# Performance work log

Measured on AMD Instinct MI355X. Metric: run time of the kernel, lower is better.

Reference implementation:

```python
import jax, jax.numpy as jnp
import numpy as np

K = 3           # kernel_size
N_LAYERS = 2    # n_layers; circuit applies StronglyEntanglingLayers(weights) N_LAYERS times
STRIDE = 2
N_QUBITS = K * K  # 9 qubits -> 512-dim statevector


def _apply_1q(state, U, q):
    """Apply 2x2 unitary U (shared (2,2) or per-batch (P,2,2)) to qubit q.
    state: (P,) + (2,)*N_QUBITS complex64."""
    s = jnp.moveaxis(state, 1 + q, -1)
    if U.ndim == 3:
        s = jnp.einsum('pji,p...i->p...j', U, s)
    else:
        s = jnp.einsum('ji,...i->...j', U, s)
    return jnp.moveaxis(s, -1, 1 + q)


def _apply_cnot(state, c, t):
    """CNOT with control c, target t on state (P,)+(2,)*n."""
    s0 = jnp.take(state, 0, axis=1 + c)
    s1 = jnp.take(state, 1, axis=1 + c)
    t_ax = 1 + t if t < c else t  # target axis after control axis removed
    s1 = jnp.flip(s1, axis=t_ax)
    return jnp.stack([s0, s1], axis=1 + c)


def _rot_matrix(phi, theta, omega):
    """PennyLane Rot(phi, theta, omega) = RZ(omega) RY(theta) RZ(phi)."""
    c = jnp.cos(theta / 2)
    s = jnp.sin(theta / 2)
    u00 = jnp.exp(-0.5j * (phi + omega)) * c
    u01 = -jnp.exp(0.5j * (phi - omega)) * s
    u10 = jnp.exp(-0.5j * (phi - omega)) * s
    u11 = jnp.exp(0.5j * (phi + omega)) * c
    return jnp.stack([jnp.stack([u00, u01]), jnp.stack([u10, u11])]).astype(jnp.complex64)


def _circuit(angles, weights):
    """angles: (P, N_QUBITS) float32. Returns PauliZ expvals (P, N_QUBITS) float32."""
    P = angles.shape[0]
    n = N_QUBITS
    state = jnp.zeros((P, 2 ** n), jnp.complex64).at[:, 0].set(1.0)
    state = state.reshape((P,) + (2,) * n)
    # AngleEmbedding (default rotation = RX) per wire, angle varies per patch
    half = angles / 2
    cos = jnp.cos(half)
    sin = jnp.sin(half)
    for q in range(n):
        c = cos[:, q].astype(jnp.complex64)
        s = (-1j * sin[:, q]).astype(jnp.complex64)
        U = jnp.stack([jnp.stack([c, s], -1), jnp.stack([s, c], -1)], -2)  # (P,2,2)
        state = _apply_1q(state, U, q)
    # Faithful to source: StronglyEntanglingLayers(weights) applied N_LAYERS times,
    # each containing N_LAYERS internal layers (Rot on each wire + CNOT ring).
    for _ in range(N_LAYERS):
        for l in range(N_LAYERS):
            for q in range(n):
                state = _apply_1q(
                    state,
                    _rot_matrix(weights[l, q, 0], weights[l, q, 1], weights[l, q, 2]),
                    q,
                )
            r = (l % (n - 1)) + 1  # PennyLane default ranges
            for q in range(n):
                state = _apply_cnot(state, q, (q + r) % n)
    probs = state.real ** 2 + state.imag ** 2  # (P,)+(2,)*n
    exps = []
    for q in range(n):
        axes = tuple(ax for ax in range(1, n + 1) if ax != 1 + q)
        m = probs.sum(axis=axes)  # (P, 2)
        exps.append(m[:, 0] - m[:, 1])
    return jnp.stack(exps, axis=1)


def _forward(input, weights):
    B, _, H, W = input.shape
    out = (H - K) // STRIDE + 1
    starts = jnp.arange(out) * STRIDE
    win = starts[:, None] + jnp.arange(K)  # (out, K) row/col start offsets
    x = input[:, 0]  # (B, H, W), channels asserted == 1
    # vectorized sliding-window patch extraction: (B, out, out, K, K)
    patches = x[:, win[:, None, :, None], win[None, :, None, :]]
    angles = patches.reshape(B * out * out, N_QUBITS)  # row-major flatten, matches torch.flatten
    ev = _circuit(angles, weights)  # (B*out*out, N_QUBITS)
    ev = ev.reshape(B, out * out, N_QUBITS).transpose(0, 2, 1)
    return ev.reshape(B, N_QUBITS, out, out).astype(jnp.float32)


def setup_inputs() -> dict:
    key = jax.random.key(0)
    k1, k2 = jax.random.split(key)
    inp = jax.random.normal(k1, (8, 1, 128, 128), dtype=jnp.float32)
    weights = jax.random.uniform(k2, (N_LAYERS, N_QUBITS, 3), dtype=jnp.float32,
                                 minval=0.0, maxval=2 * np.pi)
    return {"input": inp, "weights": weights}


def reference(input, weights):
    return _forward(input, weights)
```

## Files before the change

### kernel.cpp

```cpp
#include <hip/hip_runtime.h>


namespace {

constexpr int OUT_HW = 63;
constexpr int PPB = 4;
constexpr int N_PATCH_TOTAL = 8 * OUT_HW * OUT_HW;

typedef _Float16 h2 __attribute__((ext_vector_type(2)));
typedef __fp16  hw2 __attribute__((ext_vector_type(2)));

__device__ __forceinline__ int h2i(h2 v) { return __builtin_bit_cast(int, v); }
__device__ __forceinline__ h2  i2h(int v) { return __builtin_bit_cast(h2, v); }
__device__ __forceinline__ h2  swap_h2(h2 v) { return __builtin_shufflevector(v, v, 1, 0); }

__device__ __forceinline__ int bperm_i(int addr, int v) {
    return __builtin_amdgcn_ds_bpermute(addr, v);
}

template<int M>
__device__ __forceinline__ int shfl_i(int v, int lane) {
    if constexpr (M < 32)
        return __builtin_amdgcn_ds_swizzle(v, 0x1F | (M << 10));
    else
        return bperm_i((lane << 2) ^ 128, v);
}
template<int M>
__device__ __forceinline__ float shfl_f(float v, int lane) {
    return __int_as_float(shfl_i<M>(__float_as_int(v), lane));
}

template<int C, int T>
__device__ __forceinline__ void cnot_h(h2 (&a)[8])
{
    constexpr int cm = 1 << C, tm = 1 << T;
    #pragma unroll
    for (int r = 0; r < 8; ++r) {
        if ((r & cm) && !(r & tm)) {
            const int r1 = r | tm;
            const h2 t = a[r]; a[r] = a[r1]; a[r1] = t;
        }
    }
}

__device__ __forceinline__ void ring1_partial_h(h2 (&a)[8], int lane)
{
    cnot_h<0,1>(a);
    cnot_h<1,2>(a);
    const int sA = (lane ^ ((lane & 31) << 1)) << 2;
    const int sB = sA ^ 4;
    #pragma unroll
    for (int r = 0; r < 8; ++r)
        a[r] = i2h(bperm_i((r & 4) ? sB : sA, h2i(a[r])));
}

__device__ __forceinline__ void ring2_partial_h(h2 (&a)[8], int lane)
{
    cnot_h<0,2>(a);
    const int s0 = (lane ^ ((lane & 15) << 2)) << 2;
    #pragma unroll
    for (int r = 0; r < 8; ++r) {
        const int ad = s0 ^ (((r >> 1) & 1) << 2) ^ (((r >> 2) & 1) << 3);
        a[r] = i2h(bperm_i(ad, h2i(a[r])));
    }
}

__device__ __forceinline__ void apply_diag_h(h2 (&a)[8],
                                             const int* __restrict__ dtab,
                                             int dbase, int lane)
{
    #pragma unroll
    for (int r = 0; r < 8; ++r) {
        const int idx = (dbase + r * 64 + lane) * 2;
        const h2 cc = i2h(dtab[idx]);
        const h2 ns = i2h(dtab[idx + 1]);
        a[r] = cc * a[r] + ns * swap_h2(a[r]);
    }
}

template<int QM>
__device__ __forceinline__ void regY_h(h2 (&a)[8], h2 A2, h2 B2, h2 C2, h2 D2)
{
    #pragma unroll
    for (int r = 0; r < 8; ++r) {
        if (!(r & QM)) {
            const int r1 = r | QM;
            const h2 x0 = a[r], x1 = a[r1];
            a[r]  = A2 * x0 + B2 * x1;
            a[r1] = C2 * x0 + D2 * x1;
        }
    }
}

template<int LM>
__device__ __forceinline__ void laneY_h(h2 (&a)[8], int lane, h2 c2, h2 sp2)
{
    #pragma unroll
    for (int r = 0; r < 8; ++r) {
        const h2 p = i2h(shfl_i<LM>(h2i(a[r]), lane));
        a[r] = c2 * a[r] + sp2 * p;
    }
}

__device__ __forceinline__ void apply_Y_h(h2 (&a)[8], int lane,
                                          const int* __restrict__ yt,
                                          bool sw0, bool sw1)
{
    {   const int cc = yt[0], ss = yt[1], ns = yt[2];
        regY_h<1>(a, i2h(sw0 ? ns : cc), i2h(sw0 ? cc : ns),
                     i2h(sw0 ? cc : ss), i2h(sw0 ? ss : cc)); }
    {   const int cc = yt[3], ss = yt[4], ns = yt[5];
        regY_h<2>(a, i2h(sw1 ? ns : cc), i2h(sw1 ? cc : ns),
                     i2h(sw1 ? cc : ss), i2h(sw1 ? ss : cc)); }
    {   regY_h<4>(a, i2h(yt[6]), i2h(yt[8]), i2h(yt[7]), i2h(yt[6])); }
    {   laneY_h<1>(a, lane, i2h(yt[9]),  i2h((lane & 1)        ? yt[10] : yt[11])); }
    {   laneY_h<2>(a, lane, i2h(yt[12]), i2h(((lane >> 1) & 1) ? yt[13] : yt[14])); }
    {   laneY_h<4>(a, lane, i2h(yt[15]), i2h(((lane >> 2) & 1) ? yt[16] : yt[17])); }
    {   laneY_h<8>(a, lane, i2h(yt[18]), i2h(((lane >> 3) & 1) ? yt[19] : yt[20])); }
    {   laneY_h<16>(a, lane, i2h(yt[21]), i2h(((lane >> 4) & 1) ? yt[22] : yt[23])); }
    {   laneY_h<32>(a, lane, i2h(yt[24]), i2h(((lane >> 5) & 1) ? yt[25] : yt[26])); }
}

__global__ void precomp_kernel(const float* __restrict__ w, float* __restrict__ ws)
{
    const int tid = threadIdx.x;
    float* rot = ws;
    int* ytab = (int*)(ws + 144);
    int* dtab = (int*)(ws + 208);
    if (tid < 18) {
        const float phi = w[tid*3 + 0], theta = w[tid*3 + 1], omega = w[tid*3 + 2];
        const float ct = cosf(0.5f * theta), st = sinf(0.5f * theta);
        const float apo = 0.5f * (phi + omega), amo = 0.5f * (phi - omega);
        const float ca = cosf(apo), sa = sinf(apo);
        const float cm = cosf(amo), sm = sinf(amo);
        float* m = rot + tid * 8;
        m[0] =  ca * ct; m[1] = -sa * ct;
        m[2] = -cm * st; m[3] = -sm * st;
        m[4] =  cm * st; m[5] = -sm * st;
        m[6] =  ca * ct; m[7] =  sa * ct;
        h2 cc; cc.x = (_Float16)ct;  cc.y = (_Float16)ct;
        h2 ss; ss.x = (_Float16)st;  ss.y = (_Float16)st;
        h2 ns; ns.x = (_Float16)(-st); ns.y = (_Float16)(-st);
        ytab[tid*3 + 0] = h2i(cc);
        ytab[tid*3 + 1] = h2i(ss);
        ytab[tid*3 + 2] = h2i(ns);
    }
    if (tid < 192) {
        const int vmask[9] = {0x1FE,0x003,0x007,0x00F,0x01F,0x03F,0x07F,0x0FF,0x1FF};
        const int wmask[9] = {0x0AB,0x157,0x005,0x00A,0x015,0x02A,0x055,0x0AA,0x155};
        const int d = tid >> 6, lane = tid & 63;
        for (int r = 0; r < 8; ++r) {
            const int p = (lane << 3) | r;
            float ang = 0.f;
            for (int q = 0; q < 9; ++q) {
                if (d == 0) {
                    const float lam = -0.5f * w[(9 + q)*3 + 0];
                    ang += (__popc(p & vmask[q]) & 1) ? -lam : lam;
                } else if (d == 1) {
                    const float lam = -0.5f * w[q*3 + 0];
                    ang += (__popc(p & wmask[q]) & 1) ? -lam : lam;
                    const float lm2 = -0.5f * w[(9 + q)*3 + 2];
                    ang += ((p >> q) & 1) ? -lm2 : lm2;
                } else {
                    const float lam = -0.5f * w[(9 + q)*3 + 0];
                    ang += (__popc(p & vmask[q]) & 1) ? -lam : lam;
                    const float lm2 = -0.5f * w[q*3 + 2];
                    ang += ((p >> q) & 1) ? -lm2 : lm2;
                }
            }
            const float c = cosf(ang), s = sinf(ang);
            h2 cc;  cc.x = (_Float16)c;    cc.y = (_Float16)c;
            h2 nsp; nsp.x = (_Float16)(-s); nsp.y = (_Float16)s;
            const int idx = ((d*8 + r)*64 + lane)*2;
            dtab[idx + 0] = h2i(cc);
            dtab[idx + 1] = h2i(nsp);
        }
    }
}

__device__ __forceinline__ float sgn_apply(float v, int par) {
    return __int_as_float(__float_as_int(v) ^ (par << 31));
}

__global__ __launch_bounds__(PPB * 64, 8) void qconv_kernel(
    const float* __restrict__ x,
    const float* __restrict__ ws,
    float* __restrict__ out)
{
    const float* rot  = ws;
    const int* ytab = (const int*)(ws + 144);
    const int* dtab = (const int*)(ws + 208);

    const int lane  = threadIdx.x & 63;
    const int wv    = threadIdx.x >> 6;
    const int patch = blockIdx.x * PPB + wv;

    const int b   = patch / (OUT_HW * OUT_HW);
    const int rem = patch - b * (OUT_HW * OUT_HW);
    const int oy  = rem / OUT_HW;
    const int ox  = rem - oy * OUT_HW;

    __shared__ float abtab[PPB][36];
    {
        const int t = threadIdx.x;
        if (t < PPB * 36) {
            const int tw = t / 36, j = t - tw * 36;
            const int q = j >> 2, comp = j & 3;
            const int tp   = blockIdx.x * PPB + tw;
            const int tb   = tp / (OUT_HW * OUT_HW);
            const int trem = tp - tb * (OUT_HW * OUT_HW);
            const int toy  = trem / OUT_HW;
            const int tox  = trem - toy * OUT_HW;
            const float ang = x[tb * 16384 + (toy * 2 + q / 3) * 128 + (tox * 2 + q % 3)];
            float s, c;
            __sincosf(0.5f * ang, &s, &c);
            const float* R = rot + 8 * q;
            float v;
            if      (comp == 0) v = c*R[0] + s*R[3];
            else if (comp == 1) v = c*R[1] - s*R[2];
            else if (comp == 2) v = c*R[4] + s*R[7];
            else                v = c*R[5] - s*R[6];
            abtab[tw][j] = v;
        }
    }
    __syncthreads();

    float ab[36];
    {
        const float4* src = reinterpret_cast<const float4*>(&abtab[wv][0]);
        float4* dst = reinterpret_cast<float4*>(ab);
        #pragma unroll
        for (int j = 0; j < 9; ++j) dst[j] = src[j];
    }

    float ar[8], ai[8];
    {
        float Lr = 1.0f, Li = 0.0f;
        #pragma unroll
        for (int q = 3; q < 9; ++q) {
            const int bit = (lane >> (q - 3)) & 1;
            const float fr = bit ? ab[4*q + 2] : ab[4*q + 0];
            const float fi = bit ? ab[4*q + 3] : ab[4*q + 1];
            const float nr = Lr*fr - Li*fi;
            const float ni = Lr*fi + Li*fr;
            Lr = nr; Li = ni;
        }
        float c01r[4], c01i[4];
        #pragma unroll
        for (int j = 0; j < 4; ++j) {
            const float f0r = (j & 1) ? ab[2] : ab[0];
            const float f0i = (j & 1) ? ab[3] : ab[1];
            const float f1r = (j & 2) ? ab[6] : ab[4];
            const float f1i = (j & 2) ? ab[7] : ab[5];
            c01r[j] = f0r*f1r - f0i*f1i;
            c01i[j] = f0r*f1i + f0i*f1r;
        }
        float hr[4], hi[4];
        #pragma unroll
        for (int j = 0; j < 4; ++j) {
            hr[j] = c01r[j]*Lr - c01i[j]*Li;
            hi[j] = c01r[j]*Li + c01i[j]*Lr;
        }
        #pragma unroll
        for (int r = 0; r < 8; ++r) {
            const float f2r = (r & 4) ? ab[10] : ab[8];
            const float f2i = (r & 4) ? ab[11] : ab[9];
            ar[r] = hr[r & 3]*f2r - hi[r & 3]*f2i;
            ai[r] = hr[r & 3]*f2i + hi[r & 3]*f2r;
        }
    }

    h2 a[8];
    #pragma unroll
    for (int r = 0; r < 8; ++r)
        a[r] = __builtin_bit_cast(h2, __builtin_amdgcn_cvt_pkrtz(ar[r], ai[r]));

    const bool b4 = ((lane >> 4) & 1) != 0;
    const bool b5 = ((lane >> 5) & 1) != 0;

    apply_diag_h(a, dtab, 0 * 512, lane);
    ring1_partial_h(a, lane);
    apply_Y_h(a, lane, ytab + 27, b5, false);
    apply_diag_h(a, dtab, 1 * 512, lane);
    ring2_partial_h(a, lane);
    apply_Y_h(a, lane, ytab + 0, b4, b5);
    apply_diag_h(a, dtab, 2 * 512, lane);
    ring1_partial_h(a, lane);
    apply_Y_h(a, lane, ytab + 27, b5, false);

    float p[8];
    #pragma unroll
    for (int r = 0; r < 8; ++r) {
#if __has_builtin(__builtin_amdgcn_fdot2)
        p[r] = __builtin_amdgcn_fdot2(__builtin_bit_cast(hw2, a[r]),
                                      __builtin_bit_cast(hw2, a[r]), 0.0f, false);
#else
        const float xr = (float)a[r].x, xi = (float)a[r].y;
        p[r] = xr*xr + xi*xi;
#endif
    }

    const float t03 = p[0]+p[3], t12 = p[1]+p[2], t47 = p[4]+p[7], t56 = p[5]+p[6];
    float S3 = (t03 + t47) - (t12 + t56);
    float S7 = (t03 + t56) - (t12 + t47);
    const float u02 = p[0]+p[2], u13 = p[1]+p[3], u57 = p[5]+p[7], u46 = p[4]+p[6];
    float S5 = (u02 + u57) - (u13 + u46);
    const float v01 = p[0]+p[1], v23 = p[2]+p[3], v45 = p[4]+p[5], v67 = p[6]+p[7];
    float S2 = (v01 + v45) - (v23 + v67);

    const int sm0 = (lane & 1) << 31;
    const int sm1 = ((lane >> 1) & 1) << 31;
    const int sm2 = ((lane >> 2) & 1) << 31;
    const int sm3 = ((lane >> 3) & 1) << 31;
    const int sm4 = ((lane >> 4) & 1) << 31;
    const int sm5 = ((lane >> 5) & 1) << 31;
#define WHT_STAGE(M, SM) { \
    const float q3 = shfl_f<M>(S3, lane), q7 = shfl_f<M>(S7, lane); \
    const float q5 = shfl_f<M>(S5, lane), q2 = shfl_f<M>(S2, lane); \
    S3 = q3 + __int_as_float(__float_as_int(S3) ^ (SM)); \
    S7 = q7 + __int_as_float(__float_as_int(S7) ^ (SM)); \
    S5 = q5 + __int_as_float(__float_as_int(S5) ^ (SM)); \
    S2 = q2 + __int_as_float(__float_as_int(S2) ^ (SM)); }
    WHT_STAGE(1,  sm0)
    WHT_STAGE(2,  sm1)
    WHT_STAGE(4,  sm2)
    WHT_STAGE(8,  sm3)
    WHT_STAGE(16, sm4)
    WHT_STAGE(32, sm5)
#undef WHT_STAGE

    const int base = b * 9;
    const int pix  = oy * OUT_HW + ox;
    int chA = -1; float vA = 0.f;
    if (lane == 0x00) { chA = 2; vA = S5; }
    if (lane == 0x02) { chA = 4; vA = S5; }
    if (lane == 0x0A) { chA = 6; vA = S5; }
    if (lane == 0x2A) { chA = 8; vA = S5; }
    if (lane == 0x01) { chA = 3; vA = S2; }
    if (lane == 0x05) { chA = 5; vA = S2; }
    if (lane == 0x15) { chA = 7; vA = S2; }
    if (chA >= 0)
        out[(base + chA) * (OUT_HW * OUT_HW) + pix] = vA;
    if (lane == 0x15)
        out[(base + 0) * (OUT_HW * OUT_HW) + pix] = S3;
    if (lane == 0x2A)
        out[(base + 1) * (OUT_HW * OUT_HW) + pix] = S7;
}

}

extern "C" void kernel_launch(void* const* d_in, const int* in_sizes, int n_in,
                              void* d_out, int out_size, void* d_ws, size_t ws_size,
                              hipStream_t stream)
{
    const float* x = (const float*)d_in[0];
    const float* w = (const float*)d_in[1];
    float* ws = (float*)d_ws;
    float* out = (float*)d_out;

    precomp_kernel<<<1, 256, 0, stream>>>(w, ws);
    qconv_kernel<<<N_PATCH_TOTAL / PPB, PPB * 64, 0, stream>>>(x, ws, out);
}
```

Before: 110.0 us.

## Compute per-wave angle tables locally, use wave barrier, prefetch diagonal tables

Each wave now computes its own 36 rotation coefficients and synchronizes with a wave barrier instead of a block-wide __syncthreads. The block size drops from four to two patches per block. The next diagonal-phase table is prefetched into registers before the ring and Y stages so its global loads overlap with that compute. The cost is more registers held live, which could lower occupancy.

```diff
diff --git a/kernel.cpp b/kernel.cpp
--- a/kernel.cpp
+++ b/kernel.cpp
@@ -4,7 +4,7 @@
 namespace {
 
 constexpr int OUT_HW = 63;
-constexpr int PPB = 4;
+constexpr int PPB = 2;
 constexpr int N_PATCH_TOTAL = 8 * OUT_HW * OUT_HW;
 
 typedef _Float16 h2 __attribute__((ext_vector_type(2)));
@@ -76,6 +76,27 @@
         const h2 ns = i2h(dtab[idx + 1]);
         a[r] = cc * a[r] + ns * swap_h2(a[r]);
     }
+}
+
+__device__ __forceinline__ void load_diag(h2 (&cc)[8], h2 (&ns)[8],
+                                          const int* __restrict__ dtab,
+                                          int dbase, int lane)
+{
+    #pragma unroll
+    for (int r = 0; r < 8; ++r) {
+        const int idx = (dbase + r * 64 + lane) * 2;
+        cc[r] = i2h(dtab[idx]);
+        ns[r] = i2h(dtab[idx + 1]);
+    }
+}
+
+__device__ __forceinline__ void apply_diag_pre(h2 (&a)[8],
+                                               const h2 (&cc)[8],
+                                               const h2 (&ns)[8])
+{
+    #pragma unroll
+    for (int r = 0; r < 8; ++r)
+        a[r] = cc[r] * a[r] + ns[r] * swap_h2(a[r]);
 }
 
 template<int QM>
@@ -178,10 +199,6 @@
     }
 }
 
-__device__ __forceinline__ float sgn_apply(float v, int par) {
-    return __int_as_float(__float_as_int(v) ^ (par << 31));
-}
-
 __global__ __launch_bounds__(PPB * 64, 8) void qconv_kernel(
     const float* __restrict__ x,
     const float* __restrict__ ws,
@@ -200,30 +217,21 @@
     const int oy  = rem / OUT_HW;
     const int ox  = rem - oy * OUT_HW;
 
-    __shared__ float abtab[PPB][36];
-    {
-        const int t = threadIdx.x;
-        if (t < PPB * 36) {
-            const int tw = t / 36, j = t - tw * 36;
-            const int q = j >> 2, comp = j & 3;
-            const int tp   = blockIdx.x * PPB + tw;
-            const int tb   = tp / (OUT_HW * OUT_HW);
-            const int trem = tp - tb * (OUT_HW * OUT_HW);
-            const int toy  = trem / OUT_HW;
-            const int tox  = trem - toy * OUT_HW;
-            const float ang = x[tb * 16384 + (toy * 2 + q / 3) * 128 + (tox * 2 + q % 3)];
-            float s, c;
-            __sincosf(0.5f * ang, &s, &c);
-            const float* R = rot + 8 * q;
-            float v;
-            if      (comp == 0) v = c*R[0] + s*R[3];
-            else if (comp == 1) v = c*R[1] - s*R[2];
-            else if (comp == 2) v = c*R[4] + s*R[7];
-            else                v = c*R[5] - s*R[6];
-            abtab[tw][j] = v;
-        }
-    }
-    __syncthreads();
+    __shared__ __align__(16) float abtab[PPB][36];
+    if (lane < 36) {
+        const int q = lane >> 2, comp = lane & 3;
+        const float ang = x[b * 16384 + (oy * 2 + q / 3) * 128 + (ox * 2 + q % 3)];
+        float s, c;
+        __sincosf(0.5f * ang, &s, &c);
+        const float* R = rot + 8 * q;
+        float v;
+        if      (comp == 0) v = c*R[0] + s*R[3];
+        else if (comp == 1) v = c*R[1] - s*R[2];
+        else if (comp == 2) v = c*R[4] + s*R[7];
+        else                v = c*R[5] - s*R[6];
+        abtab[wv][lane] = v;
+    }
+    __builtin_amdgcn_wave_barrier();
 
     float ab[36];
     {
@@ -278,13 +286,16 @@
     const bool b4 = ((lane >> 4) & 1) != 0;
     const bool b5 = ((lane >> 5) & 1) != 0;
 
+    h2 dcc[8], dns[8];
     apply_diag_h(a, dtab, 0 * 512, lane);
+    load_diag(dcc, dns, dtab, 1 * 512, lane);
     ring1_partial_h(a, lane);
     apply_Y_h(a, lane, ytab + 27, b5, false);
-    apply_diag_h(a, dtab, 1 * 512, lane);
+    apply_diag_pre(a, dcc, dns);
+    load_diag(dcc, dns, dtab, 2 * 512, lane);
     ring2_partial_h(a, lane);
     apply_Y_h(a, lane, ytab + 0, b4, b5);
-    apply_diag_h(a, dtab, 2 * 512, lane);
+    apply_diag_pre(a, dcc, dns);
     ring1_partial_h(a, lane);
     apply_Y_h(a, lane, ytab + 27, b5, false);
 
```

Result: no change. 112.2 us (+1.9%).

## Pack two patches per wavefront with 16 amplitudes per lane

Applied to the files above, without the earlier changes.

Each 64-lane wavefront now simulates two patches, one per 32-lane half, and each lane holds 16 amplitudes instead of 8. Qubit-to-lane/register mappings, CNOT permutations, the diagonal-table layout, the Walsh-Hadamard reduction and the output lane selection are all remapped to match. The block-wide barrier becomes a wave barrier. The aim is to halve the number of wavefronts and cut cross-lane shuffles per amplitude. The cost is more registers per lane and lower occupancy (launch bounds reduced to 4), plus the risk of errors in the remapped qubit indexing.

```diff
diff --git a/kernel.cpp b/kernel.cpp
--- a/kernel.cpp
+++ b/kernel.cpp
@@ -4,8 +4,9 @@
 namespace {
 
 constexpr int OUT_HW = 63;
-constexpr int PPB = 4;
-constexpr int N_PATCH_TOTAL = 8 * OUT_HW * OUT_HW;
+constexpr int N_PIX = OUT_HW * OUT_HW;
+constexpr int PPB = 2;
+constexpr int N_PATCH_TOTAL = 8 * N_PIX;
 
 typedef _Float16 h2 __attribute__((ext_vector_type(2)));
 typedef __fp16  hw2 __attribute__((ext_vector_type(2)));
@@ -31,11 +32,11 @@
 }
 
 template<int C, int T>
-__device__ __forceinline__ void cnot_h(h2 (&a)[8])
+__device__ __forceinline__ void cnot16(h2 (&a)[16])
 {
     constexpr int cm = 1 << C, tm = 1 << T;
     #pragma unroll
-    for (int r = 0; r < 8; ++r) {
+    for (int r = 0; r < 16; ++r) {
         if ((r & cm) && !(r & tm)) {
             const int r1 = r | tm;
             const h2 t = a[r]; a[r] = a[r1]; a[r1] = t;
@@ -43,46 +44,51 @@
     }
 }
 
-__device__ __forceinline__ void ring1_partial_h(h2 (&a)[8], int lane)
-{
-    cnot_h<0,1>(a);
-    cnot_h<1,2>(a);
-    const int sA = (lane ^ ((lane & 31) << 1)) << 2;
+__device__ __forceinline__ void ring1_partial16(h2 (&a)[16], int lane)
+{
+    cnot16<0,1>(a);
+    cnot16<1,2>(a);
+    cnot16<2,3>(a);
+    const int l5 = lane & 31;
+    const int hi = (lane & 32) << 2;
+    const int sA = ((l5 ^ ((l5 & 15) << 1)) << 2) | hi;
     const int sB = sA ^ 4;
     #pragma unroll
-    for (int r = 0; r < 8; ++r)
-        a[r] = i2h(bperm_i((r & 4) ? sB : sA, h2i(a[r])));
-}
-
-__device__ __forceinline__ void ring2_partial_h(h2 (&a)[8], int lane)
-{
-    cnot_h<0,2>(a);
-    const int s0 = (lane ^ ((lane & 15) << 2)) << 2;
-    #pragma unroll
-    for (int r = 0; r < 8; ++r) {
-        const int ad = s0 ^ (((r >> 1) & 1) << 2) ^ (((r >> 2) & 1) << 3);
+    for (int r = 0; r < 16; ++r)
+        a[r] = i2h(bperm_i((r & 8) ? sB : sA, h2i(a[r])));
+}
+
+__device__ __forceinline__ void ring2_partial16(h2 (&a)[16], int lane)
+{
+    cnot16<0,2>(a);
+    cnot16<1,3>(a);
+    const int l5 = lane & 31;
+    const int s0 = ((l5 ^ ((l5 & 7) << 2)) << 2) | ((lane & 32) << 2);
+    #pragma unroll
+    for (int r = 0; r < 16; ++r) {
+        const int ad = s0 ^ (((r >> 3) & 1) << 3) ^ (((r >> 2) & 1) << 2);
         a[r] = i2h(bperm_i(ad, h2i(a[r])));
     }
 }
 
-__device__ __forceinline__ void apply_diag_h(h2 (&a)[8],
+__device__ __forceinline__ void apply_diag16(h2 (&a)[16],
                                              const int* __restrict__ dtab,
-                                             int dbase, int lane)
-{
-    #pragma unroll
-    for (int r = 0; r < 8; ++r) {
-        const int idx = (dbase + r * 64 + lane) * 2;
-        const h2 cc = i2h(dtab[idx]);
-        const h2 ns = i2h(dtab[idx + 1]);
+                                             int dbase, int lane5)
+{
+    const int* dp = dtab + (dbase + (lane5 << 4)) * 2;
+    #pragma unroll
+    for (int r = 0; r < 16; ++r) {
+        const h2 cc = i2h(dp[2 * r]);
+        const h2 ns = i2h(dp[2 * r + 1]);
         a[r] = cc * a[r] + ns * swap_h2(a[r]);
     }
 }
 
 template<int QM>
-__device__ __forceinline__ void regY_h(h2 (&a)[8], h2 A2, h2 B2, h2 C2, h2 D2)
-{
-    #pragma unroll
-    for (int r = 0; r < 8; ++r) {
+__device__ __forceinline__ void regY16(h2 (&a)[16], h2 A2, h2 B2, h2 C2, h2 D2)
+{
+    #pragma unroll
+    for (int r = 0; r < 16; ++r) {
         if (!(r & QM)) {
             const int r1 = r | QM;
             const h2 x0 = a[r], x1 = a[r1];
@@ -93,32 +99,32 @@
 }
 
 template<int LM>
-__device__ __forceinline__ void laneY_h(h2 (&a)[8], int lane, h2 c2, h2 sp2)
-{
-    #pragma unroll
-    for (int r = 0; r < 8; ++r) {
+__device__ __forceinline__ void laneY16(h2 (&a)[16], int lane, h2 c2, h2 sp2)
+{
+    #pragma unroll
+    for (int r = 0; r < 16; ++r) {
         const h2 p = i2h(shfl_i<LM>(h2i(a[r]), lane));
         a[r] = c2 * a[r] + sp2 * p;
     }
 }
 
-__device__ __forceinline__ void apply_Y_h(h2 (&a)[8], int lane,
+__device__ __forceinline__ void apply_Y16(h2 (&a)[16], int lane,
                                           const int* __restrict__ yt,
                                           bool sw0, bool sw1)
 {
     {   const int cc = yt[0], ss = yt[1], ns = yt[2];
-        regY_h<1>(a, i2h(sw0 ? ns : cc), i2h(sw0 ? cc : ns),
+        regY16<1>(a, i2h(sw0 ? ns : cc), i2h(sw0 ? cc : ns),
                      i2h(sw0 ? cc : ss), i2h(sw0 ? ss : cc)); }
     {   const int cc = yt[3], ss = yt[4], ns = yt[5];
-        regY_h<2>(a, i2h(sw1 ? ns : cc), i2h(sw1 ? cc : ns),
+        regY16<2>(a, i2h(sw1 ? ns : cc), i2h(sw1 ? cc : ns),
                      i2h(sw1 ? cc : ss), i2h(sw1 ? ss : cc)); }
-    {   regY_h<4>(a, i2h(yt[6]), i2h(yt[8]), i2h(yt[7]), i2h(yt[6])); }
-    {   laneY_h<1>(a, lane, i2h(yt[9]),  i2h((lane & 1)        ? yt[10] : yt[11])); }
-    {   laneY_h<2>(a, lane, i2h(yt[12]), i2h(((lane >> 1) & 1) ? yt[13] : yt[14])); }
-    {   laneY_h<4>(a, lane, i2h(yt[15]), i2h(((lane >> 2) & 1) ? yt[16] : yt[17])); }
-    {   laneY_h<8>(a, lane, i2h(yt[18]), i2h(((lane >> 3) & 1) ? yt[19] : yt[20])); }
-    {   laneY_h<16>(a, lane, i2h(yt[21]), i2h(((lane >> 4) & 1) ? yt[22] : yt[23])); }
-    {   laneY_h<32>(a, lane, i2h(yt[24]), i2h(((lane >> 5) & 1) ? yt[25] : yt[26])); }
+    {   regY16<4>(a, i2h(yt[6]),  i2h(yt[8]),  i2h(yt[7]),  i2h(yt[6])); }
+    {   regY16<8>(a, i2h(yt[9]),  i2h(yt[11]), i2h(yt[10]), i2h(yt[9])); }
+    {   laneY16<1> (a, lane, i2h(yt[12]), i2h((lane & 1)        ? yt[13] : yt[14])); }
+    {   laneY16<2> (a, lane, i2h(yt[15]), i2h(((lane >> 1) & 1) ? yt[16] : yt[17])); }
+    {   laneY16<4> (a, lane, i2h(yt[18]), i2h(((lane >> 2) & 1) ? yt[19] : yt[20])); }
+    {   laneY16<8> (a, lane, i2h(yt[21]), i2h(((lane >> 3) & 1) ? yt[22] : yt[23])); }
+    {   laneY16<16>(a, lane, i2h(yt[24]), i2h(((lane >> 4) & 1) ? yt[25] : yt[26])); }
 }
 
 __global__ void precomp_kernel(const float* __restrict__ w, float* __restrict__ ws)
@@ -148,9 +154,9 @@
     if (tid < 192) {
         const int vmask[9] = {0x1FE,0x003,0x007,0x00F,0x01F,0x03F,0x07F,0x0FF,0x1FF};
         const int wmask[9] = {0x0AB,0x157,0x005,0x00A,0x015,0x02A,0x055,0x0AA,0x155};
-        const int d = tid >> 6, lane = tid & 63;
+        const int d = tid >> 6, ln = tid & 63;
         for (int r = 0; r < 8; ++r) {
-            const int p = (lane << 3) | r;
+            const int p = (ln << 3) | r;
             float ang = 0.f;
             for (int q = 0; q < 9; ++q) {
                 if (d == 0) {
@@ -171,18 +177,14 @@
             const float c = cosf(ang), s = sinf(ang);
             h2 cc;  cc.x = (_Float16)c;    cc.y = (_Float16)c;
             h2 nsp; nsp.x = (_Float16)(-s); nsp.y = (_Float16)s;
-            const int idx = ((d*8 + r)*64 + lane)*2;
+            const int idx = (d * 512 + p) * 2;
             dtab[idx + 0] = h2i(cc);
             dtab[idx + 1] = h2i(nsp);
         }
     }
 }
 
-__device__ __forceinline__ float sgn_apply(float v, int par) {
-    return __int_as_float(__float_as_int(v) ^ (par << 31));
-}
-
-__global__ __launch_bounds__(PPB * 64, 8) void qconv_kernel(
+__global__ __launch_bounds__(PPB * 64, 4) void qconv_kernel(
     const float* __restrict__ x,
     const float* __restrict__ ws,
     float* __restrict__ out)
@@ -191,27 +193,23 @@
     const int* ytab = (const int*)(ws + 144);
     const int* dtab = (const int*)(ws + 208);
 
-    const int lane  = threadIdx.x & 63;
-    const int wv    = threadIdx.x >> 6;
-    const int patch = blockIdx.x * PPB + wv;
-
-    const int b   = patch / (OUT_HW * OUT_HW);
-    const int rem = patch - b * (OUT_HW * OUT_HW);
-    const int oy  = rem / OUT_HW;
-    const int ox  = rem - oy * OUT_HW;
-
-    __shared__ float abtab[PPB][36];
+    const int lane   = threadIdx.x & 63;
+    const int wv     = threadIdx.x >> 6;
+    const int lane5  = lane & 31;
+    const int half   = lane >> 5;
+    const int patch2 = (blockIdx.x * PPB + wv) * 2;
+
+    __shared__ __align__(16) float abtab[PPB][2][36];
     {
-        const int t = threadIdx.x;
-        if (t < PPB * 36) {
-            const int tw = t / 36, j = t - tw * 36;
+        auto stage_val = [&](int h, int j) {
             const int q = j >> 2, comp = j & 3;
-            const int tp   = blockIdx.x * PPB + tw;
-            const int tb   = tp / (OUT_HW * OUT_HW);
-            const int trem = tp - tb * (OUT_HW * OUT_HW);
+            const int tp   = patch2 + h;
+            const int tb   = tp / N_PIX;
+            const int trem = tp - tb * N_PIX;
             const int toy  = trem / OUT_HW;
             const int tox  = trem - toy * OUT_HW;
-            const float ang = x[tb * 16384 + (toy * 2 + q / 3) * 128 + (tox * 2 + q % 3)];
+            const int qr = q / 3, qc = q - 3 * qr;
+            const float ang = x[tb * 16384 + (toy * 2 + qr) * 128 + (tox * 2 + qc)];
             float s, c;
             __sincosf(0.5f * ang, &s, &c);
             const float* R = rot + 8 * q;
@@ -220,77 +218,85 @@
             else if (comp == 1) v = c*R[1] - s*R[2];
             else if (comp == 2) v = c*R[4] + s*R[7];
             else                v = c*R[5] - s*R[6];
-            abtab[tw][j] = v;
-        }
-    }
-    __syncthreads();
+            abtab[wv][h][j] = v;
+        };
+        const int h1 = (lane >= 36) ? 1 : 0;
+        stage_val(h1, lane - 36 * h1);
+        if (lane < 8) stage_val(1, 28 + lane);
+    }
+    __builtin_amdgcn_wave_barrier();
 
     float ab[36];
     {
-        const float4* src = reinterpret_cast<const float4*>(&abtab[wv][0]);
+        const float4* src = reinterpret_cast<const float4*>(&abtab[wv][half][0]);
         float4* dst = reinterpret_cast<float4*>(ab);
         #pragma unroll
         for (int j = 0; j < 9; ++j) dst[j] = src[j];
     }
 
-    float ar[8], ai[8];
+    h2 a[16];
     {
-        float Lr = 1.0f, Li = 0.0f;
-        #pragma unroll
-        for (int q = 3; q < 9; ++q) {
-            const int bit = (lane >> (q - 3)) & 1;
+        float Lr, Li;
+        {
+            const int bit = lane5 & 1;
+            Lr = ab[16 + (bit ? 2 : 0)];
+            Li = ab[16 + (bit ? 3 : 1)];
+        }
+        #pragma unroll
+        for (int q = 5; q <= 8; ++q) {
+            const int bit = (lane5 >> (q - 4)) & 1;
             const float fr = bit ? ab[4*q + 2] : ab[4*q + 0];
             const float fi = bit ? ab[4*q + 3] : ab[4*q + 1];
             const float nr = Lr*fr - Li*fi;
             const float ni = Lr*fi + Li*fr;
             Lr = nr; Li = ni;
         }
-        float c01r[4], c01i[4];
+        float c01r[4], c01i[4], c23r[4], c23i[4];
         #pragma unroll
         for (int j = 0; j < 4; ++j) {
-            const float f0r = (j & 1) ? ab[2] : ab[0];
-            const float f0i = (j & 1) ? ab[3] : ab[1];
-            const float f1r = (j & 2) ? ab[6] : ab[4];
-            const float f1i = (j & 2) ? ab[7] : ab[5];
+            const float f0r = (j & 1) ? ab[2]  : ab[0];
+            const float f0i = (j & 1) ? ab[3]  : ab[1];
+            const float f1r = (j & 2) ? ab[6]  : ab[4];
+            const float f1i = (j & 2) ? ab[7]  : ab[5];
             c01r[j] = f0r*f1r - f0i*f1i;
             c01i[j] = f0r*f1i + f0i*f1r;
-        }
-        float hr[4], hi[4];
+            const float g2r = (j & 1) ? ab[10] : ab[8];
+            const float g2i = (j & 1) ? ab[11] : ab[9];
+            const float g3r = (j & 2) ? ab[14] : ab[12];
+            const float g3i = (j & 2) ? ab[15] : ab[13];
+            c23r[j] = g2r*g3r - g2i*g3i;
+            c23i[j] = g2r*g3i + g2i*g3r;
+        }
+        float hlr[4], hli[4];
         #pragma unroll
         for (int j = 0; j < 4; ++j) {
-            hr[j] = c01r[j]*Lr - c01i[j]*Li;
-            hi[j] = c01r[j]*Li + c01i[j]*Lr;
-        }
-        #pragma unroll
-        for (int r = 0; r < 8; ++r) {
-            const float f2r = (r & 4) ? ab[10] : ab[8];
-            const float f2i = (r & 4) ? ab[11] : ab[9];
-            ar[r] = hr[r & 3]*f2r - hi[r & 3]*f2i;
-            ai[r] = hr[r & 3]*f2i + hi[r & 3]*f2r;
-        }
-    }
-
-    h2 a[8];
-    #pragma unroll
-    for (int r = 0; r < 8; ++r)
-        a[r] = __builtin_bit_cast(h2, __builtin_amdgcn_cvt_pkrtz(ar[r], ai[r]));
-
-    const bool b4 = ((lane >> 4) & 1) != 0;
-    const bool b5 = ((lane >> 5) & 1) != 0;
-
-    apply_diag_h(a, dtab, 0 * 512, lane);
-    ring1_partial_h(a, lane);
-    apply_Y_h(a, lane, ytab + 27, b5, false);
-    apply_diag_h(a, dtab, 1 * 512, lane);
-    ring2_partial_h(a, lane);
-    apply_Y_h(a, lane, ytab + 0, b4, b5);
-    apply_diag_h(a, dtab, 2 * 512, lane);
-    ring1_partial_h(a, lane);
-    apply_Y_h(a, lane, ytab + 27, b5, false);
-
-    float p[8];
-    #pragma unroll
-    for (int r = 0; r < 8; ++r) {
+            hlr[j] = c01r[j]*Lr - c01i[j]*Li;
+            hli[j] = c01r[j]*Li + c01i[j]*Lr;
+        }
+        #pragma unroll
+        for (int r = 0; r < 16; ++r) {
+            const float fr = hlr[r & 3]*c23r[r >> 2] - hli[r & 3]*c23i[r >> 2];
+            const float fi = hlr[r & 3]*c23i[r >> 2] + hli[r & 3]*c23r[r >> 2];
+            a[r] = __builtin_bit_cast(h2, __builtin_amdgcn_cvt_pkrtz(fr, fi));
+        }
+    }
+
+    const bool q7b = ((lane >> 3) & 1) != 0;
+    const bool q8b = ((lane >> 4) & 1) != 0;
+
+    apply_diag16(a, dtab, 0 * 512, lane5);
+    ring1_partial16(a, lane);
+    apply_Y16(a, lane, ytab + 27, q8b, false);
+    apply_diag16(a, dtab, 1 * 512, lane5);
+    ring2_partial16(a, lane);
+    apply_Y16(a, lane, ytab + 0, q7b, q8b);
+    apply_diag16(a, dtab, 2 * 512, lane5);
+    ring1_partial16(a, lane);
+    apply_Y16(a, lane, ytab + 27, q8b, false);
+
+    float p[16];
+    #pragma unroll
+    for (int r = 0; r < 16; ++r) {
 #if __has_builtin(__builtin_amdgcn_fdot2)
         p[r] = __builtin_amdgcn_fdot2(__builtin_bit_cast(hw2, a[r]),
                                       __builtin_bit_cast(hw2, a[r]), 0.0f, false);
@@ -300,51 +306,66 @@
 #endif
     }
 
-    const float t03 = p[0]+p[3], t12 = p[1]+p[2], t47 = p[4]+p[7], t56 = p[5]+p[6];
-    float S3 = (t03 + t47) - (t12 + t56);
-    float S7 = (t03 + t56) - (t12 + t47);
-    const float u02 = p[0]+p[2], u13 = p[1]+p[3], u57 = p[5]+p[7], u46 = p[4]+p[6];
-    float S5 = (u02 + u57) - (u13 + u46);
-    const float v01 = p[0]+p[1], v23 = p[2]+p[3], v45 = p[4]+p[5], v67 = p[6]+p[7];
-    float S2 = (v01 + v45) - (v23 + v67);
+    float A[8], B[8];
+    #pragma unroll
+    for (int j = 0; j < 8; ++j) {
+        A[j] = p[2*j] + p[2*j+1];
+        B[j] = p[2*j] - p[2*j+1];
+    }
+    float P5[4], P7[4], P10[4];
+    #pragma unroll
+    for (int k = 0; k < 4; ++k) {
+        P5[k]  = B[2*k] + B[2*k+1];
+        P7[k]  = B[2*k] - B[2*k+1];
+        P10[k] = A[2*k] - A[2*k+1];
+    }
+    float S5  = (P5[0]  - P5[1])  + (P5[2]  - P5[3]);
+    float S7  = (P7[0]  - P7[1])  + (P7[2]  - P7[3]);
+    float S11 = (P7[0]  + P7[1])  - (P7[2]  + P7[3]);
+    float S10 = (P10[0] + P10[1]) - (P10[2] + P10[3]);
 
     const int sm0 = (lane & 1) << 31;
     const int sm1 = ((lane >> 1) & 1) << 31;
     const int sm2 = ((lane >> 2) & 1) << 31;
     const int sm3 = ((lane >> 3) & 1) << 31;
     const int sm4 = ((lane >> 4) & 1) << 31;
-    const int sm5 = ((lane >> 5) & 1) << 31;
 #define WHT_STAGE(M, SM) { \
-    const float q3 = shfl_f<M>(S3, lane), q7 = shfl_f<M>(S7, lane); \
-    const float q5 = shfl_f<M>(S5, lane), q2 = shfl_f<M>(S2, lane); \
-    S3 = q3 + __int_as_float(__float_as_int(S3) ^ (SM)); \
-    S7 = q7 + __int_as_float(__float_as_int(S7) ^ (SM)); \
-    S5 = q5 + __int_as_float(__float_as_int(S5) ^ (SM)); \
-    S2 = q2 + __int_as_float(__float_as_int(S2) ^ (SM)); }
+    const float qa = shfl_f<M>(S5, lane),  qb = shfl_f<M>(S7, lane); \
+    const float qc = shfl_f<M>(S10, lane), qd = shfl_f<M>(S11, lane); \
+    S5  = qa + __int_as_float(__float_as_int(S5)  ^ (SM)); \
+    S7  = qb + __int_as_float(__float_as_int(S7)  ^ (SM)); \
+    S10 = qc + __int_as_float(__float_as_int(S10) ^ (SM)); \
+    S11 = qd + __int_as_float(__float_as_int(S11) ^ (SM)); }
     WHT_STAGE(1,  sm0)
     WHT_STAGE(2,  sm1)
     WHT_STAGE(4,  sm2)
     WHT_STAGE(8,  sm3)
     WHT_STAGE(16, sm4)
-    WHT_STAGE(32, sm5)
 #undef WHT_STAGE
 
+    const int patch = patch2 + half;
+    const int b   = patch / N_PIX;
+    const int rem = patch - b * N_PIX;
+    const int oy  = rem / OUT_HW;
+    const int ox  = rem - oy * OUT_HW;
     const int base = b * 9;
     const int pix  = oy * OUT_HW + ox;
-    int chA = -1; float vA = 0.f;
-    if (lane == 0x00) { chA = 2; vA = S5; }
-    if (lane == 0x02) { chA = 4; vA = S5; }
-    if (lane == 0x0A) { chA = 6; vA = S5; }
-    if (lane == 0x2A) { chA = 8; vA = S5; }
-    if (lane == 0x01) { chA = 3; vA = S2; }
-    if (lane == 0x05) { chA = 5; vA = S2; }
-    if (lane == 0x15) { chA = 7; vA = S2; }
-    if (chA >= 0)
-        out[(base + chA) * (OUT_HW * OUT_HW) + pix] = vA;
-    if (lane == 0x15)
-        out[(base + 0) * (OUT_HW * OUT_HW) + pix] = S3;
-    if (lane == 0x2A)
-        out[(base + 1) * (OUT_HW * OUT_HW) + pix] = S7;
+
+    if (lane5 == 0x00) {
+        out[(base + 2) * N_PIX + pix] = S5;
+        out[(base + 3) * N_PIX + pix] = S10;
+    }
+    if (lane5 == 0x01) out[(base + 4) * N_PIX + pix] = S5;
+    if (lane5 == 0x02) out[(base + 5) * N_PIX + pix] = S10;
+    if (lane5 == 0x05) out[(base + 6) * N_PIX + pix] = S5;
+    if (lane5 == 0x0A) {
+        out[(base + 7) * N_PIX + pix] = S10;
+        out[(base + 0) * N_PIX + pix] = S11;
+    }
+    if (lane5 == 0x15) {
+        out[(base + 8) * N_PIX + pix] = S5;
+        out[(base + 1) * N_PIX + pix] = S7;
+    }
 }
 
 }
@@ -359,5 +380,5 @@
     float* out = (float*)d_out;
 
     precomp_kernel<<<1, 256, 0, stream>>>(w, ws);
-    qconv_kernel<<<N_PATCH_TOTAL / PPB, PPB * 64, 0, stream>>>(x, ws, out);
-}
+    qconv_kernel<<<N_PATCH_TOTAL / (PPB * 2), PPB * 64, 0, stream>>>(x, ws, out);
+}
```

Measured after the change: 142.1 us. +29.1%, slower.
